# Kernel tuning notes

Measured on AMD Instinct MI355X. Metric: run time of the kernel, lower is better.

The kernel has to match this reference:

```python
import jax, jax.numpy as jnp
import numpy as np

NUM_HEADS = 16
HIDDEN = 1024
B, S = 2, 2048


def setup_inputs() -> dict:
    key = jax.random.key(0)
    ks = jax.random.split(key, 14)
    D = HIDDEN
    scale = 1.0 / np.sqrt(D)
    inp = {
        "query": jax.random.normal(ks[0], (B, S, D), jnp.float32),
        "key_in": jax.random.normal(ks[1], (B, S, D), jnp.float32),
        "value": jax.random.normal(ks[2], (B, S, D), jnp.float32),
        "group_prob": jax.random.uniform(ks[3], (B, S, S), jnp.float32),
        "mask": jax.random.randint(ks[4], (B, S, S), 0, 2, jnp.int32),
        "wq_k": jax.random.normal(ks[5], (D, D), jnp.float32) * scale,
        "wq_b": jnp.zeros((D,), jnp.float32),
        "wk_k": jax.random.normal(ks[6], (D, D), jnp.float32) * scale,
        "wk_b": jnp.zeros((D,), jnp.float32),
        "wv_k": jax.random.normal(ks[7], (D, D), jnp.float32) * scale,
        "wv_b": jnp.zeros((D,), jnp.float32),
        "wo_k": jax.random.normal(ks[8], (D, D), jnp.float32) * scale,
        "wo_b": jnp.zeros((D,), jnp.float32),
    }
    return inp


def _split_heads(x, H):
    b, s, d = x.shape
    return x.reshape(b, s, H, d // H).transpose(0, 2, 1, 3)  # (B,H,S,dh)


def reference(query, key_in, value, group_prob, mask,
              wq_k, wq_b, wk_k, wk_b, wv_k, wv_b, wo_k, wo_b):
    H = NUM_HEADS
    dh = query.shape[-1] // H
    q = _split_heads(query @ wq_k + wq_b, H)
    k = _split_heads(key_in @ wk_k + wk_b, H)
    v = _split_heads(value @ wv_k + wv_b, H)
    # scaled dot-product logits (B,H,Sq,Sk)
    logits = jnp.einsum('bhqd,bhkd->bhqk', q, k) / jnp.sqrt(jnp.asarray(dh, q.dtype))
    neg = (1.0 - mask.astype(q.dtype)) * -1e9
    logits = logits + neg[:, None, :, :]
    attn = jax.nn.softmax(logits, axis=-1)
    # Tree Transformer modulation: post-softmax elementwise scale by group_prob
    attn = attn * group_prob[:, None, :, :]
    out = jnp.einsum('bhqk,bhkd->bhqd', attn, v)
    out = out.transpose(0, 2, 1, 3).reshape(query.shape[0], -1, H * dh)
    return out @ wo_k + wo_b
```

## Files before the change

### kernel.cpp

```cpp
#include <hip/hip_runtime.h>
#include <hip/hip_bf16.h>
#include <stdint.h>

#define B_ 2
#define S_ 2048
#define D_ 1024
#define H_ 16
#define DH 64

typedef __attribute__((ext_vector_type(4))) float f32x4;
typedef __attribute__((ext_vector_type(8))) short s16x8;
typedef __attribute__((ext_vector_type(4))) short s16x4;

__device__ inline short f2bf(float f) {
  union { float f; unsigned u; } v; v.f = f;
  unsigned r = (v.u + 0x7fffu + ((v.u >> 16) & 1u)) >> 16;
  return (short)r;
}

__device__ inline float bfbits_lo(unsigned u) {
  union { unsigned x; float f; } v; v.x = u << 16; return v.f;
}
__device__ inline float bfbits_hi(unsigned u) {
  union { unsigned x; float f; } v; v.x = u & 0xffff0000u; return v.f;
}

__device__ inline float exp2v(float x) {
  float r; asm("v_exp_f32 %0, %1" : "=v"(r) : "v"(x)); return r;
}
__device__ inline unsigned cvtpk(float a, float b) {
  unsigned r; asm("v_cvt_pk_bf16_f32 %0, %1, %2" : "=v"(r) : "v"(a), "v"(b));
  return r;
}

__global__ __launch_bounds__(256) void cvt3_f32_bf16(const float* __restrict__ a,
                                                     const float* __restrict__ b,
                                                     const float* __restrict__ c,
                                                     short* oa, short* ob, short* oc,
                                                     int n) {
  int z = blockIdx.y;
  const float* in = z == 0 ? a : (z == 1 ? b : c);
  short* out = z == 0 ? oa : (z == 1 ? ob : oc);
  int i = (blockIdx.x * 256 + threadIdx.x) * 4;
  if (i < n) {
    float4 v = *(const float4*)(in + i);
    s16x4 o;
    o.x = f2bf(v.x); o.y = f2bf(v.y); o.z = f2bf(v.z); o.w = f2bf(v.w);
    *(s16x4*)(out + i) = o;
  }
}

__global__ __launch_bounds__(256) void transpose_cvt4(
    const float* __restrict__ i0, const float* __restrict__ i1,
    const float* __restrict__ i2, const float* __restrict__ i3,
    short* o0, short* o1, short* o2, short* o3) {
  int z = blockIdx.z;
  const float* in = z == 0 ? i0 : (z == 1 ? i1 : (z == 2 ? i2 : i3));
  short* out = z == 0 ? o0 : (z == 1 ? o1 : (z == 2 ? o2 : o3));
  __shared__ float tile[32][33];
  int bx = blockIdx.x, by = blockIdx.y;
  int x = bx * 32 + threadIdx.x;
#pragma unroll
  for (int i = 0; i < 32; i += 8) {
    int y = by * 32 + threadIdx.y + i;
    tile[threadIdx.y + i][threadIdx.x] = in[(size_t)y * D_ + x];
  }
  __syncthreads();
  int ox = by * 32 + threadIdx.x;
#pragma unroll
  for (int i = 0; i < 32; i += 8) {
    int oy = bx * 32 + threadIdx.y + i;
    out[(size_t)oy * D_ + ox] = f2bf(tile[threadIdx.x][threadIdx.y + i]);
  }
}

#define FUSE_BLK ((B_ * S_ * S_) / 1024)
__global__ __launch_bounds__(256) void prep_attn(const int* __restrict__ mask,
                                                 const float* __restrict__ gp,
                                                 short* __restrict__ mgp,
                                                 const short* __restrict__ vp,
                                                 short* __restrict__ vt) {
  __shared__ __align__(16) short t[64 * 72];
  int bid = blockIdx.x;
  int tid = threadIdx.x;
  if (bid < FUSE_BLK) {
    int i = (bid * 256 + tid) * 4;
    int4 m = *(const int4*)(mask + i);
    float4 g = *(const float4*)(gp + i);
    short b0 = f2bf(g.x); if (!b0) b0 = (short)0x0080;
    short b1 = f2bf(g.y); if (!b1) b1 = (short)0x0080;
    short b2 = f2bf(g.z); if (!b2) b2 = (short)0x0080;
    short b3 = f2bf(g.w); if (!b3) b3 = (short)0x0080;
    s16x4 o;
    o.x = m.x ? b0 : 0;
    o.y = m.y ? b1 : 0;
    o.z = m.z ? b2 : 0;
    o.w = m.w ? b3 : 0;
    *(s16x4*)(mgp + i) = o;
  } else {
    int l = bid - FUSE_BLK;
    int s0 = (l & 31) * 64;
    int bh = l >> 5, b = bh >> 4, h = bh & 15;
    int r = tid >> 2, cc = tid & 3;
    const short* src = vp + ((size_t)(b * S_ + s0 + r)) * D_ + h * DH + cc * 16;
    s16x8 a = *(const s16x8*)src;
    s16x8 bb = *(const s16x8*)(src + 8);
    int pc = (cc ^ (r >> 4)) * 16;
    *(s16x8*)&t[r * 72 + pc] = a;
    *(s16x8*)&t[r * 72 + pc + 8] = bb;
    __syncthreads();
    int d = tid >> 2, sc = (tid & 3) * 16;
    s16x8 o0, o1;
#pragma unroll
    for (int j = 0; j < 8; ++j) {
      int row = sc + j;
      o0[j] = t[row * 72 + ((d >> 4) ^ (row >> 4)) * 16 + (d & 15)];
      int row2 = sc + 8 + j;
      o1[j] = t[row2 * 72 + ((d >> 4) ^ (row2 >> 4)) * 16 + (d & 15)];
    }
    short* dst = vt + ((size_t)(b * H_ + h) * DH + d) * S_ + s0 + sc;
    *(s16x8*)dst = o0;
    *(s16x8*)(dst + 8) = o1;
  }
}

__device__ inline void gload_lds16(const void* g, void* l) {
  __builtin_amdgcn_global_load_lds(
      (const __attribute__((address_space(1))) unsigned*)g,
      (__attribute__((address_space(3))) unsigned*)l, 16, 0, 0);
}

#define BM 128
#define BN 128
#define BK 32

__global__ __launch_bounds__(256) void gemm_bt3(
    const short* __restrict__ A0, const short* __restrict__ A1, const short* __restrict__ A2,
    const short* __restrict__ Bt0, const short* __restrict__ Bt1, const short* __restrict__ Bt2,
    const float* __restrict__ bs0, const float* __restrict__ bs1, const float* __restrict__ bs2,
    void* C0, void* C1, void* C2,
    int M, int N, int K, int f32out, float os0, float os1, float os2) {
  int z = blockIdx.y;
  const short* A = z == 0 ? A0 : (z == 1 ? A1 : A2);
  const short* Bt = z == 0 ? Bt0 : (z == 1 ? Bt1 : Bt2);
  const float* bias = z == 0 ? bs0 : (z == 1 ? bs1 : bs2);
  void* C = z == 0 ? C0 : (z == 1 ? C1 : C2);
  float oscale = z == 0 ? os0 : (z == 1 ? os1 : os2);

  __shared__ __align__(16) short As[BM * BK];
  __shared__ __align__(16) short Bs[BN * BK];
  int tid = threadIdx.x;
  int lane = tid & 63, wave = tid >> 6;
  int l15 = lane & 15, l4 = lane >> 4;
  int ntn = N / BN;
  int bid = blockIdx.x;
  bid = ((bid & 7) << 5) | (bid >> 3);
  int bm = bid / ntn, bn = bid % ntn;
  int row0 = bm * BM, col0 = bn * BN;
  int wm = (wave >> 1) * 64, wn = (wave & 1) * 64;

  f32x4 acc[4][4] = {};

  for (int k0 = 0; k0 < K; k0 += BK) {
    __syncthreads();
#pragma unroll
    for (int it = 0; it < 2; ++it) {
      int ch = it * 256 + tid;
      int r = ch >> 2, c = (ch & 3) * 8;
      int ldsbase = (it * 256 + wave * 64) * 8;
      gload_lds16(A + (size_t)(row0 + r) * K + k0 + c, &As[ldsbase]);
      gload_lds16(Bt + (size_t)(col0 + r) * K + k0 + c, &Bs[ldsbase]);
    }
    __syncthreads();
    s16x8 af[4], bf[4];
#pragma unroll
    for (int mf = 0; mf < 4; ++mf)
      af[mf] = *(const s16x8*)&As[(wm + mf * 16 + l15) * BK + l4 * 8];
#pragma unroll
    for (int nf = 0; nf < 4; ++nf)
      bf[nf] = *(const s16x8*)&Bs[(wn + nf * 16 + l15) * BK + l4 * 8];
#pragma unroll
    for (int mf = 0; mf < 4; ++mf)
#pragma unroll
      for (int nf = 0; nf < 4; ++nf)
        acc[mf][nf] = __builtin_amdgcn_mfma_f32_16x16x32_bf16(af[mf], bf[nf],
                                                              acc[mf][nf], 0, 0, 0);
  }

#pragma unroll
  for (int nf = 0; nf < 4; ++nf) {
    int gcol = col0 + wn + nf * 16 + l15;
    float bv = bias[gcol];
#pragma unroll
    for (int mf = 0; mf < 4; ++mf) {
#pragma unroll
      for (int r = 0; r < 4; ++r) {
        int grow = row0 + wm + mf * 16 + l4 * 4 + r;
        float v = (acc[mf][nf][r] + bv) * oscale;
        if (f32out)
          ((float*)C)[(size_t)grow * N + gcol] = v;
        else
          ((short*)C)[(size_t)grow * N + gcol] = f2bf(v);
      }
    }
  }
}

#define QB 128
#define NB 64
#define NTILES (S_ / NB)
#define M0_SHIFT 12.0f

__global__ __launch_bounds__(256, 3) void attn_fused(const short* __restrict__ Qp,
                                                     const short* __restrict__ Kp,
                                                     const short* __restrict__ VT,
                                                     const short* __restrict__ MGP,
                                                     short* __restrict__ ctx) {
  __shared__ __align__(16) short Ks[2][64 * 64];
  __shared__ __align__(16) short Vs[2][64 * 64];
  __shared__ __align__(16) short Ps[4][32 * 64];

  int tid = threadIdx.x, lane = tid & 63, wave = tid >> 6;
  int l15 = lane & 15, l4 = lane >> 4;
  int q0 = blockIdx.x * QB;
  int bh = blockIdx.y;
  int b = bh >> 4, h = bh & 15;
  int wq = wave * 32;

  const short* Qbase = Qp + (size_t)b * S_ * D_ + (size_t)h * DH;
  const short* Kbase = Kp + (size_t)b * S_ * D_ + (size_t)h * DH;
  const short* Vbase = VT + (size_t)(b * H_ + h) * DH * S_;
  const short* Mrow0 = MGP + (size_t)b * S_ * S_ + (size_t)(q0 + wq + l15) * S_ + l4 * 4;
  const short* Mrow1 = Mrow0 + (size_t)16 * S_;

  int i0 = tid, i1 = 256 + tid;
  int r0 = i0 >> 3, c0 = (i0 & 7) ^ (r0 & 7);
  int r1 = i1 >> 3, c1 = (i1 & 7) ^ (r1 & 7);
  int ldsA = wave * 512;
  int ldsB = 2048 + wave * 512;

#define STAGE(kv0, buf)                                                       \
  do {                                                                        \
    gload_lds16(Kbase + (size_t)((kv0) + r0) * D_ + c0 * 8, &Ks[buf][ldsA]);  \
    gload_lds16(Kbase + (size_t)((kv0) + r1) * D_ + c1 * 8, &Ks[buf][ldsB]);  \
    gload_lds16(Vbase + (size_t)r0 * S_ + (kv0) + c0 * 8, &Vs[buf][ldsA]);    \
    gload_lds16(Vbase + (size_t)r1 * S_ + (kv0) + c1 * 8, &Vs[buf][ldsB]);    \
  } while (0)

  s16x8 qf[2][2];
#pragma unroll
  for (int mf = 0; mf < 2; ++mf)
#pragma unroll
    for (int ks = 0; ks < 2; ++ks)
      qf[mf][ks] = *(const s16x8*)(Qbase + (size_t)(q0 + wq + mf * 16 + l15) * D_ +
                                   ks * 32 + l4 * 8);

  float lsum[2] = {0.f, 0.f};
  f32x4 oacc[2][4] = {};

  STAGE(0, 0);

  int q7 = l15 & 7;
  short* Pw = &Ps[wave][0];
  int prow[2] = {l15 * 64, (16 + l15) * 64};

  for (int t = 0; t < NTILES; ++t) {
    int buf = t & 1;
    int kvt = t * NB;

    uint2 g2[2][4];
#pragma unroll
    for (int nf = 0; nf < 4; ++nf) {
      g2[0][nf] = *(const uint2*)(Mrow0 + kvt + nf * 16);
      g2[1][nf] = *(const uint2*)(Mrow1 + kvt + nf * 16);
    }
    __builtin_amdgcn_sched_barrier(0);
    if (t + 1 < NTILES) {
      STAGE((t + 1) * NB, buf ^ 1);
      __builtin_amdgcn_sched_barrier(0);
      asm volatile("s_waitcnt vmcnt(12)" ::: "memory");
    } else {
      __builtin_amdgcn_sched_barrier(0);
      asm volatile("s_waitcnt vmcnt(8)" ::: "memory");
    }
    __builtin_amdgcn_s_barrier();
    __builtin_amdgcn_sched_barrier(0);

    f32x4 sacc[2][4] = {};
    __builtin_amdgcn_s_setprio(1);
#pragma unroll
    for (int nf = 0; nf < 4; ++nf) {
      int R = nf * 16 + l15;
#pragma unroll
      for (int ks = 0; ks < 2; ++ks) {
        s16x8 kf = *(const s16x8*)&Ks[buf][R * 64 + (((ks * 4 + l4) ^ q7) * 8)];
#pragma unroll
        for (int mf = 0; mf < 2; ++mf)
          sacc[mf][nf] = __builtin_amdgcn_mfma_f32_16x16x32_bf16(kf, qf[mf][ks],
                                                                 sacc[mf][nf], 0, 0, 0);
      }
    }
    __builtin_amdgcn_s_setprio(0);

    float ee[2][4][4];
#pragma unroll
    for (int mf = 0; mf < 2; ++mf)
#pragma unroll
      for (int nf = 0; nf < 4; ++nf)
#pragma unroll
        for (int r = 0; r < 4; ++r)
          ee[mf][nf][r] = exp2v(sacc[mf][nf][r] - M0_SHIFT);

    if (t + 1 < NTILES)
      asm volatile("s_waitcnt vmcnt(4)" ::: "memory");
    else
      asm volatile("s_waitcnt vmcnt(0)" ::: "memory");
    __builtin_amdgcn_sched_barrier(0);

#pragma unroll
    for (int mf = 0; mf < 2; ++mf) {
#pragma unroll
      for (int nf = 0; nf < 4; ++nf) {
        float gv0 = bfbits_lo(g2[mf][nf].x), gv1 = bfbits_hi(g2[mf][nf].x);
        float gv2 = bfbits_lo(g2[mf][nf].y), gv3 = bfbits_hi(g2[mf][nf].y);
        float e0 = ee[mf][nf][0], e1 = ee[mf][nf][1];
        float e2 = ee[mf][nf][2], e3 = ee[mf][nf][3];
        lsum[mf] += (gv0 != 0.f) ? e0 : 0.f;
        lsum[mf] += (gv1 != 0.f) ? e1 : 0.f;
        lsum[mf] += (gv2 != 0.f) ? e2 : 0.f;
        lsum[mf] += (gv3 != 0.f) ? e3 : 0.f;
        uint2 wp;
        wp.x = cvtpk(e0 * gv0, e1 * gv1);
        wp.y = cvtpk(e2 * gv2, e3 * gv3);
        int gr = ((nf * 2 + (l4 >> 1)) ^ q7) * 8 + (l4 & 1) * 4;
        *(uint2*)&Pw[prow[mf] + gr] = wp;
      }
    }

    __builtin_amdgcn_s_setprio(1);
#pragma unroll
    for (int ks = 0; ks < 2; ++ks) {
      s16x8 pa[2];
#pragma unroll
      for (int mf = 0; mf < 2; ++mf)
        pa[mf] = *(const s16x8*)&Pw[prow[mf] + (((ks * 4 + l4) ^ q7) * 8)];
#pragma unroll
      for (int df = 0; df < 4; ++df) {
        s16x8 vf = *(const s16x8*)&Vs[buf][(df * 16 + l15) * 64 +
                                           (((ks * 4 + l4) ^ q7) * 8)];
#pragma unroll
        for (int mf = 0; mf < 2; ++mf)
          oacc[mf][df] = __builtin_amdgcn_mfma_f32_16x16x32_bf16(vf, pa[mf],
                                                                 oacc[mf][df], 0, 0, 0);
      }
    }
    __builtin_amdgcn_s_setprio(0);

    asm volatile("s_waitcnt lgkmcnt(0)" ::: "memory");
    __builtin_amdgcn_s_barrier();
  }
#undef STAGE

#pragma unroll
  for (int mf = 0; mf < 2; ++mf) {
    float ls = lsum[mf];
    ls += __shfl_xor(ls, 16);
    ls += __shfl_xor(ls, 32);
    float inv = 1.f / ls;
    short* crow = ctx + ((size_t)(b * S_ + q0 + wq + mf * 16 + l15)) * D_ + h * DH;
#pragma unroll
    for (int df = 0; df < 4; ++df) {
      uint2 o;
      o.x = cvtpk(oacc[mf][df][0] * inv, oacc[mf][df][1] * inv);
      o.y = cvtpk(oacc[mf][df][2] * inv, oacc[mf][df][3] * inv);
      *(uint2*)(crow + df * 16 + l4 * 4) = o;
    }
  }
}

extern "C" void kernel_launch(void* const* d_in, const int* in_sizes, int n_in,
                              void* d_out, int out_size, void* d_ws, size_t ws_size,
                              hipStream_t stream) {
  const float* query = (const float*)d_in[0];
  const float* key_in = (const float*)d_in[1];
  const float* value = (const float*)d_in[2];
  const float* group_prob = (const float*)d_in[3];
  const int* mask = (const int*)d_in[4];
  const float* wq_k = (const float*)d_in[5];
  const float* wq_b = (const float*)d_in[6];
  const float* wk_k = (const float*)d_in[7];
  const float* wk_b = (const float*)d_in[8];
  const float* wv_k = (const float*)d_in[9];
  const float* wv_b = (const float*)d_in[10];
  const float* wo_k = (const float*)d_in[11];
  const float* wo_b = (const float*)d_in[12];
  float* out = (float*)d_out;

  short* ws = (short*)d_ws;
  const size_t NT = (size_t)B_ * S_ * D_;
  short* qbf = ws;
  short* kbf = qbf + NT;
  short* vbf = kbf + NT;
  short* wqt = vbf + NT;
  short* wkt = wqt + (size_t)D_ * D_;
  short* wvt = wkt + (size_t)D_ * D_;
  short* wot = wvt + (size_t)D_ * D_;
  short* qp = wot + (size_t)D_ * D_;
  short* kp = qp + NT;
  short* vp = kp + NT;
  short* ctx = vp + NT;
  short* mgp = ws;
  short* vt = vbf;

  int nblk = (int)(NT / 4 / 256);
  cvt3_f32_bf16<<<dim3(nblk, 3), 256, 0, stream>>>(query, key_in, value,
                                                   qbf, kbf, vbf, (int)NT);

  dim3 tb(32, 8);
  transpose_cvt4<<<dim3(D_ / 32, D_ / 32, 4), tb, 0, stream>>>(
      wq_k, wk_k, wv_k, wo_k, wqt, wkt, wvt, wot);

  int M = B_ * S_;
  int gblocks = (M / BM) * (D_ / BN);
  const float QSCALE = 0.125f * 1.4426950408889634f;
  gemm_bt3<<<dim3(gblocks, 3), 256, 0, stream>>>(
      qbf, kbf, vbf, wqt, wkt, wvt, wq_b, wk_b, wv_b, qp, kp, vp,
      M, D_, D_, 0, QSCALE, 1.0f, 1.0f);

  prep_attn<<<FUSE_BLK + (S_ / 64) * B_ * H_, 256, 0, stream>>>(
      mask, group_prob, mgp, vp, vt);

  dim3 ag(S_ / QB, B_ * H_);
  attn_fused<<<ag, 256, 0, stream>>>(qp, kp, vt, mgp, ctx);

  gemm_bt3<<<dim3(gblocks, 1), 256, 0, stream>>>(
      ctx, ctx, ctx, wot, wot, wot, wo_b, wo_b, wo_b, out, out, out,
      M, D_, D_, 1, 1.0f, 1.0f, 1.0f);
}
```

Baseline: 181.0 us.

## Fuse mask and group_prob preprocessing into the attention kernel

```diff
diff --git a/kernel.cpp b/kernel.cpp
--- a/kernel.cpp
+++ b/kernel.cpp
@@ -16,13 +16,6 @@
   union { float f; unsigned u; } v; v.f = f;
   unsigned r = (v.u + 0x7fffu + ((v.u >> 16) & 1u)) >> 16;
   return (short)r;
-}
-
-__device__ inline float bfbits_lo(unsigned u) {
-  union { unsigned x; float f; } v; v.x = u << 16; return v.f;
-}
-__device__ inline float bfbits_hi(unsigned u) {
-  union { unsigned x; float f; } v; v.x = u & 0xffff0000u; return v.f;
 }
 
 __device__ inline float exp2v(float x) {
@@ -74,54 +67,32 @@
   }
 }
 
-#define FUSE_BLK ((B_ * S_ * S_) / 1024)
-__global__ __launch_bounds__(256) void prep_attn(const int* __restrict__ mask,
-                                                 const float* __restrict__ gp,
-                                                 short* __restrict__ mgp,
-                                                 const short* __restrict__ vp,
-                                                 short* __restrict__ vt) {
+__global__ __launch_bounds__(256) void transpose_v(const short* __restrict__ vp,
+                                                   short* __restrict__ vt) {
   __shared__ __align__(16) short t[64 * 72];
-  int bid = blockIdx.x;
   int tid = threadIdx.x;
-  if (bid < FUSE_BLK) {
-    int i = (bid * 256 + tid) * 4;
-    int4 m = *(const int4*)(mask + i);
-    float4 g = *(const float4*)(gp + i);
-    short b0 = f2bf(g.x); if (!b0) b0 = (short)0x0080;
-    short b1 = f2bf(g.y); if (!b1) b1 = (short)0x0080;
-    short b2 = f2bf(g.z); if (!b2) b2 = (short)0x0080;
-    short b3 = f2bf(g.w); if (!b3) b3 = (short)0x0080;
-    s16x4 o;
-    o.x = m.x ? b0 : 0;
-    o.y = m.y ? b1 : 0;
-    o.z = m.z ? b2 : 0;
-    o.w = m.w ? b3 : 0;
-    *(s16x4*)(mgp + i) = o;
-  } else {
-    int l = bid - FUSE_BLK;
-    int s0 = (l & 31) * 64;
-    int bh = l >> 5, b = bh >> 4, h = bh & 15;
-    int r = tid >> 2, cc = tid & 3;
-    const short* src = vp + ((size_t)(b * S_ + s0 + r)) * D_ + h * DH + cc * 16;
-    s16x8 a = *(const s16x8*)src;
-    s16x8 bb = *(const s16x8*)(src + 8);
-    int pc = (cc ^ (r >> 4)) * 16;
-    *(s16x8*)&t[r * 72 + pc] = a;
-    *(s16x8*)&t[r * 72 + pc + 8] = bb;
-    __syncthreads();
-    int d = tid >> 2, sc = (tid & 3) * 16;
-    s16x8 o0, o1;
-#pragma unroll
-    for (int j = 0; j < 8; ++j) {
-      int row = sc + j;
-      o0[j] = t[row * 72 + ((d >> 4) ^ (row >> 4)) * 16 + (d & 15)];
-      int row2 = sc + 8 + j;
-      o1[j] = t[row2 * 72 + ((d >> 4) ^ (row2 >> 4)) * 16 + (d & 15)];
-    }
-    short* dst = vt + ((size_t)(b * H_ + h) * DH + d) * S_ + s0 + sc;
-    *(s16x8*)dst = o0;
-    *(s16x8*)(dst + 8) = o1;
-  }
+  int bh = blockIdx.y, b = bh >> 4, h = bh & 15;
+  int s0 = blockIdx.x * 64;
+  int r = tid >> 2, cc = tid & 3;
+  const short* src = vp + ((size_t)(b * S_ + s0 + r)) * D_ + h * DH + cc * 16;
+  s16x8 a = *(const s16x8*)src;
+  s16x8 bb = *(const s16x8*)(src + 8);
+  int pc = (cc ^ (r >> 4)) * 16;
+  *(s16x8*)&t[r * 72 + pc] = a;
+  *(s16x8*)&t[r * 72 + pc + 8] = bb;
+  __syncthreads();
+  int d = tid >> 2, sc = (tid & 3) * 16;
+  s16x8 o0, o1;
+#pragma unroll
+  for (int j = 0; j < 8; ++j) {
+    int row = sc + j;
+    o0[j] = t[row * 72 + ((d >> 4) ^ (row >> 4)) * 16 + (d & 15)];
+    int row2 = sc + 8 + j;
+    o1[j] = t[row2 * 72 + ((d >> 4) ^ (row2 >> 4)) * 16 + (d & 15)];
+  }
+  short* dst = vt + ((size_t)(b * H_ + h) * DH + d) * S_ + s0 + sc;
+  *(s16x8*)dst = o0;
+  *(s16x8*)(dst + 8) = o1;
 }
 
 __device__ inline void gload_lds16(const void* g, void* l) {
@@ -211,10 +182,11 @@
 #define NTILES (S_ / NB)
 #define M0_SHIFT 12.0f
 
-__global__ __launch_bounds__(256, 3) void attn_fused(const short* __restrict__ Qp,
+__global__ __launch_bounds__(256, 2) void attn_fused(const short* __restrict__ Qp,
                                                      const short* __restrict__ Kp,
                                                      const short* __restrict__ VT,
-                                                     const short* __restrict__ MGP,
+                                                     const int* __restrict__ mask,
+                                                     const float* __restrict__ gp,
                                                      short* __restrict__ ctx) {
   __shared__ __align__(16) short Ks[2][64 * 64];
   __shared__ __align__(16) short Vs[2][64 * 64];
@@ -230,8 +202,11 @@
   const short* Qbase = Qp + (size_t)b * S_ * D_ + (size_t)h * DH;
   const short* Kbase = Kp + (size_t)b * S_ * D_ + (size_t)h * DH;
   const short* Vbase = VT + (size_t)(b * H_ + h) * DH * S_;
-  const short* Mrow0 = MGP + (size_t)b * S_ * S_ + (size_t)(q0 + wq + l15) * S_ + l4 * 4;
-  const short* Mrow1 = Mrow0 + (size_t)16 * S_;
+  size_t rowbase = ((size_t)b * S_ + (size_t)(q0 + wq + l15)) * S_ + l4 * 4;
+  const int* MK0 = mask + rowbase;
+  const int* MK1 = MK0 + (size_t)16 * S_;
+  const float* GP0 = gp + rowbase;
+  const float* GP1 = GP0 + (size_t)16 * S_;
 
   int i0 = tid, i1 = 256 + tid;
   int r0 = i0 >> 3, c0 = (i0 & 7) ^ (r0 & 7);
@@ -268,20 +243,23 @@
     int buf = t & 1;
     int kvt = t * NB;
 
-    uint2 g2[2][4];
+    int4 mk[2][4];
+    float4 gpv[2][4];
 #pragma unroll
     for (int nf = 0; nf < 4; ++nf) {
-      g2[0][nf] = *(const uint2*)(Mrow0 + kvt + nf * 16);
-      g2[1][nf] = *(const uint2*)(Mrow1 + kvt + nf * 16);
+      mk[0][nf] = *(const int4*)(MK0 + kvt + nf * 16);
+      mk[1][nf] = *(const int4*)(MK1 + kvt + nf * 16);
+      gpv[0][nf] = *(const float4*)(GP0 + kvt + nf * 16);
+      gpv[1][nf] = *(const float4*)(GP1 + kvt + nf * 16);
     }
     __builtin_amdgcn_sched_barrier(0);
     if (t + 1 < NTILES) {
       STAGE((t + 1) * NB, buf ^ 1);
       __builtin_amdgcn_sched_barrier(0);
-      asm volatile("s_waitcnt vmcnt(12)" ::: "memory");
+      asm volatile("s_waitcnt vmcnt(20)" ::: "memory");
     } else {
       __builtin_amdgcn_sched_barrier(0);
-      asm volatile("s_waitcnt vmcnt(8)" ::: "memory");
+      asm volatile("s_waitcnt vmcnt(16)" ::: "memory");
     }
     __builtin_amdgcn_s_barrier();
     __builtin_amdgcn_sched_barrier(0);
@@ -321,14 +299,18 @@
     for (int mf = 0; mf < 2; ++mf) {
 #pragma unroll
       for (int nf = 0; nf < 4; ++nf) {
-        float gv0 = bfbits_lo(g2[mf][nf].x), gv1 = bfbits_hi(g2[mf][nf].x);
-        float gv2 = bfbits_lo(g2[mf][nf].y), gv3 = bfbits_hi(g2[mf][nf].y);
+        int4 m4 = mk[mf][nf];
+        float4 g4 = gpv[mf][nf];
+        float gv0 = m4.x ? g4.x : 0.f;
+        float gv1 = m4.y ? g4.y : 0.f;
+        float gv2 = m4.z ? g4.z : 0.f;
+        float gv3 = m4.w ? g4.w : 0.f;
         float e0 = ee[mf][nf][0], e1 = ee[mf][nf][1];
         float e2 = ee[mf][nf][2], e3 = ee[mf][nf][3];
-        lsum[mf] += (gv0 != 0.f) ? e0 : 0.f;
-        lsum[mf] += (gv1 != 0.f) ? e1 : 0.f;
-        lsum[mf] += (gv2 != 0.f) ? e2 : 0.f;
-        lsum[mf] += (gv3 != 0.f) ? e3 : 0.f;
+        lsum[mf] += m4.x ? e0 : 0.f;
+        lsum[mf] += m4.y ? e1 : 0.f;
+        lsum[mf] += m4.z ? e2 : 0.f;
+        lsum[mf] += m4.w ? e3 : 0.f;
         uint2 wp;
         wp.x = cvtpk(e0 * gv0, e1 * gv1);
         wp.y = cvtpk(e2 * gv2, e3 * gv3);
@@ -409,7 +391,6 @@
   short* kp = qp + NT;
   short* vp = kp + NT;
   short* ctx = vp + NT;
-  short* mgp = ws;
   short* vt = vbf;
 
   int nblk = (int)(NT / 4 / 256);
@@ -427,11 +408,10 @@
       qbf, kbf, vbf, wqt, wkt, wvt, wq_b, wk_b, wv_b, qp, kp, vp,
       M, D_, D_, 0, QSCALE, 1.0f, 1.0f);
 
-  prep_attn<<<FUSE_BLK + (S_ / 64) * B_ * H_, 256, 0, stream>>>(
-      mask, group_prob, mgp, vp, vt);
+  transpose_v<<<dim3(S_ / 64, B_ * H_), 256, 0, stream>>>(vp, vt);
 
   dim3 ag(S_ / QB, B_ * H_);
-  attn_fused<<<ag, 256, 0, stream>>>(qp, kp, vt, mgp, ctx);
+  attn_fused<<<ag, 256, 0, stream>>>(qp, kp, vt, mask, group_prob, ctx);
 
   gemm_bt3<<<dim3(gblocks, 1), 256, 0, stream>>>(
       ctx, ctx, ctx, wot, wot, wot, wo_b, wo_b, wo_b, out, out, out,
```

New measurement: 252.1 us. 39.3% more time.
